# Kernel tuning notes

Measured on AMD Instinct MI355X. Metric: run time of the kernel, lower is better.

The kernel has to match this reference:

```python
import jax, jax.numpy as jnp
import numpy as np
import math

MSG_K = 256  # min(active_count, 256); with uniform(0,1) activations active_count >> 256
N_HEADS = 4
LN_EPS = 1e-5


def _mha(x, wi, bi, wo, bo):
    # torch nn.MultiheadAttention self-attention, batch_first=True
    B, K, D = x.shape
    H = N_HEADS
    hd = D // H
    qkv = x @ wi.T + bi                      # [B,K,3D]
    q, k, v = jnp.split(qkv, 3, axis=-1)
    def split_heads(t):
        return t.reshape(B, K, H, hd).transpose(0, 2, 1, 3)  # [B,H,K,hd]
    q, k, v = split_heads(q), split_heads(k), split_heads(v)
    scores = jnp.einsum('bhqd,bhkd->bhqk', q, k) * (1.0 / math.sqrt(hd))
    attn = jax.nn.softmax(scores, axis=-1)
    o = jnp.einsum('bhqk,bhkd->bhqd', attn, v)
    o = o.transpose(0, 2, 1, 3).reshape(B, K, D)
    return o @ wo.T + bo


def _layernorm(x, g, b):
    mu = jnp.mean(x, axis=-1, keepdims=True)
    var = jnp.mean((x - mu) ** 2, axis=-1, keepdims=True)
    return (x - mu) * jax.lax.rsqrt(var + LN_EPS) * g + b


def setup_inputs() -> dict:
    key = jax.random.key(0)
    ks = jax.random.split(key, 12)
    B, N, D = 32, 4096, 256
    s = 0.02
    return {
        'activation': jax.random.uniform(ks[0], (B, N), dtype=jnp.float32),
        'hidden_state': jax.random.normal(ks[1], (B, N, D), dtype=jnp.float32),
        'in_proj_w': jax.random.normal(ks[2], (3 * D, D), dtype=jnp.float32) * s,
        'in_proj_b': jnp.zeros((3 * D,), jnp.float32),
        'out_proj_w': jax.random.normal(ks[3], (D, D), dtype=jnp.float32) * s,
        'out_proj_b': jnp.zeros((D,), jnp.float32),
        'su_w1': jax.random.normal(ks[4], (D, 2 * D), dtype=jnp.float32) * s,
        'su_b1': jnp.zeros((D,), jnp.float32),
        'su_w2': jax.random.normal(ks[5], (D, D), dtype=jnp.float32) * s,
        'su_b2': jnp.zeros((D,), jnp.float32),
        'au_w1': jax.random.normal(ks[6], (D, 2 * D), dtype=jnp.float32) * s,
        'au_b1': jnp.zeros((D,), jnp.float32),
        'au_w2': jax.random.normal(ks[7], (1, D), dtype=jnp.float32) * s,
        'au_b2': jnp.zeros((1,), jnp.float32),
        'ln_g': jnp.ones((D,), jnp.float32),
        'ln_b': jnp.zeros((D,), jnp.float32),
        'sparsity_k': 256,
    }


def reference(activation, hidden_state, in_proj_w, in_proj_b, out_proj_w, out_proj_b,
              su_w1, su_b1, su_w2, su_b2, au_w1, au_b1, au_w2, au_b2, ln_g, ln_b,
              sparsity_k):
    B, N, D = hidden_state.shape
    b_idx = jnp.arange(B)[:, None]

    # ---- compute_messages: top-k gather -> sparse MHA -> scatter back ----
    topk_vals, topk_idx = jax.lax.top_k(activation, MSG_K)        # [B,K]
    active_states = jnp.take_along_axis(hidden_state, topk_idx[..., None], axis=1)  # [B,K,D]
    msg_sparse = _mha(active_states, in_proj_w, in_proj_b, out_proj_w, out_proj_b)
    msg_sparse = msg_sparse * topk_vals[..., None]
    messages = jnp.zeros((B, N, D), hidden_state.dtype).at[b_idx, topk_idx].set(msg_sparse)

    # ---- update_states: MLP on [old, messages] + LayerNorm ----
    combined = jnp.concatenate([hidden_state, messages], axis=-1)  # [B,N,2D]
    h = jax.nn.gelu(combined @ su_w1.T + su_b1, approximate=False)
    new_hidden = _layernorm(h @ su_w2.T + su_b2, ln_g, ln_b)

    # ---- update_activations ----
    comb2 = jnp.concatenate([hidden_state, new_hidden], axis=-1)
    h2 = jax.nn.gelu(comb2 @ au_w1.T + au_b1, approximate=False)
    delta = jax.nn.sigmoid((h2 @ au_w2.T + au_b2).squeeze(-1))     # [B,N]
    new_activation = jnp.clip(0.7 * activation + 0.3 * delta, 0.0, 1.0)

    # ---- maintain_sparsity: keep top sparsity_k, zero the rest ----
    k = min(int(sparsity_k), N)
    tv, ti = jax.lax.top_k(new_activation, k)                      # [B,k]
    sparse_act = jnp.zeros_like(new_activation).at[b_idx, ti].set(tv)
    kept_hidden = jnp.take_along_axis(new_hidden, ti[..., None], axis=1)
    sparse_hidden = jnp.zeros_like(new_hidden).at[b_idx, ti].set(kept_hidden)
    return sparse_act, sparse_hidden
```

## Files before the change

### kernel.cpp

```cpp
#include <hip/hip_runtime.h>


constexpr int KC = 32;
constexpr int CMAX = 2304;
constexpr float BAND_EPS = 0.004f;
constexpr int MAXBAND = 512;

typedef short bf16x8 __attribute__((ext_vector_type(8)));
typedef float f32x4 __attribute__((ext_vector_type(4)));

__device__ __forceinline__ float gelu_f(float x) {
    return 0.5f * x * (1.0f + erff(x * 0.70710678118654752440f));
}
__device__ __forceinline__ unsigned short f2bf(float f) {
    unsigned u = __float_as_uint(f);
    return (unsigned short)((u + 0x7fffu + ((u >> 16) & 1u)) >> 16);
}
__device__ __forceinline__ float bf2f(unsigned short h) {
    return __uint_as_float(((unsigned)h) << 16);
}
__device__ __forceinline__ int swz(int row, int byteInRow) {
    return (row << 9) + (byteInRow ^ ((row & 7) << 4));
}

__global__ void __launch_bounds__(256) fill0_k(float4* p, long n4) {
    long i = (long)blockIdx.x * 256 + threadIdx.x;
    long stride = (long)gridDim.x * 256;
    float4 z = make_float4(0.f, 0.f, 0.f, 0.f);
    for (; i < n4; i += stride) p[i] = z;
}

__global__ void __launch_bounds__(256) topk1_k(const float* __restrict__ act,
        float* __restrict__ svals, int* __restrict__ sidx, int* __restrict__ cnt)
{
    __shared__ int cs[4];
    __shared__ int sTop, sRest;
    int b = blockIdx.x, tid = threadIdx.x;
    int wid = tid >> 6, lane = tid & 63;
    unsigned v[16];
    #pragma unroll
    for (int s = 0; s < 16; ++s)
        v[s] = __float_as_uint(act[b * 4096 + s * 256 + tid]);

    auto reduce4 = [&](int c) -> int {
        #pragma unroll
        for (int off = 32; off >= 1; off >>= 1) c += __shfl_xor(c, off);
        if (lane == 0) cs[wid] = c;
        __syncthreads();
        int tot = cs[0] + cs[1] + cs[2] + cs[3];
        __syncthreads();
        return tot;
    };
    auto countGE = [&](unsigned thr) -> int {
        int c = 0;
        #pragma unroll
        for (int s = 0; s < 16; ++s) c += (v[s] >= thr) ? 1 : 0;
        return reduce4(c);
    };
    auto countEqLt = [&](unsigned vs, int icut) -> int {
        int c = 0;
        #pragma unroll
        for (int s = 0; s < 16; ++s)
            c += (v[s] == vs && (s * 256 + tid) < icut) ? 1 : 0;
        return reduce4(c);
    };

    unsigned vstar = 0;
    for (int bit = 31; bit >= 0; --bit) {
        unsigned cand = vstar | (1u << bit);
        if (countGE(cand) >= 256) vstar = cand;
    }
    int cgt = countGE(vstar + 1);
    int needed = 256 - cgt;
    int icut = 4096;
    if (countEqLt(vstar, 4096) > needed) {
        int lo = 0, hi = 4096;
        for (int it = 0; it < 12; ++it) {
            int mid = (lo + hi) >> 1;
            if (countEqLt(vstar, mid) <= needed) lo = mid; else hi = mid;
        }
        icut = lo;
    }
    if (tid == 0) { sTop = 0; sRest = 0; }
    __syncthreads();
    float th = __uint_as_float(vstar) - 0.4288f;
    #pragma unroll
    for (int s = 0; s < 16; ++s) {
        int i = s * 256 + tid;
        unsigned vb = v[s];
        float f = __uint_as_float(vb);
        bool top = (vb > vstar) || (vb == vstar && i < icut);
        if (top) {
            int slot = atomicAdd(&sTop, 1);
            sidx[b * 4096 + slot] = i;
            svals[b * 4096 + slot] = f;
        } else if (f >= th) {
            int slot = 256 + atomicAdd(&sRest, 1);
            if (slot < CMAX) {
                sidx[b * 4096 + slot] = i;
                svals[b * 4096 + slot] = f;
            }
        }
    }
    __syncthreads();
    if (tid == 0) cnt[b] = min(256 + sRest, CMAX);
}

__global__ void __launch_bounds__(256) topk2_k(const float* __restrict__ newact,
        const int* __restrict__ sidx, const int* __restrict__ cnt,
        float* __restrict__ selv, int* __restrict__ selo, int* __restrict__ selp)
{
    __shared__ int cs[4];
    __shared__ int sSel;
    int b = blockIdx.x, tid = threadIdx.x;
    int wid = tid >> 6, lane = tid & 63;
    int C = min(cnt[b], CMAX);
    unsigned v[9];
    int org[9];
    #pragma unroll
    for (int s = 0; s < 9; ++s) {
        int p = s * 256 + tid;
        bool ok = (p < C && p < CMAX);
        v[s] = ok ? __float_as_uint(newact[(long)b * CMAX + p]) : 0u;
        org[s] = ok ? sidx[b * 4096 + p] : 0x7FFFFFFF;
    }
    auto reduce4 = [&](int c) -> int {
        #pragma unroll
        for (int off = 32; off >= 1; off >>= 1) c += __shfl_xor(c, off);
        if (lane == 0) cs[wid] = c;
        __syncthreads();
        int tot = cs[0] + cs[1] + cs[2] + cs[3];
        __syncthreads();
        return tot;
    };
    auto countGE = [&](unsigned thr) -> int {
        int c = 0;
        #pragma unroll
        for (int s = 0; s < 9; ++s) c += (v[s] >= thr) ? 1 : 0;
        return reduce4(c);
    };
    auto countEqLt = [&](unsigned vs, int icut) -> int {
        int c = 0;
        #pragma unroll
        for (int s = 0; s < 9; ++s) c += (v[s] == vs && org[s] < icut) ? 1 : 0;
        return reduce4(c);
    };

    unsigned vstar = 0;
    for (int bit = 31; bit >= 0; --bit) {
        unsigned cand = vstar | (1u << bit);
        if (countGE(cand) >= 256) vstar = cand;
    }
    int cgt = countGE(vstar + 1);
    int needed = 256 - cgt;
    int icut = 4096;
    if (countEqLt(vstar, 4096) > needed) {
        int lo = 0, hi = 4096;
        for (int it = 0; it < 12; ++it) {
            int mid = (lo + hi) >> 1;
            if (countEqLt(vstar, mid) <= needed) lo = mid; else hi = mid;
        }
        icut = lo;
    }
    if (tid == 0) sSel = 0;
    __syncthreads();
    #pragma unroll
    for (int s = 0; s < 9; ++s) {
        unsigned vb = v[s];
        bool sel = (vb > vstar) || (vb == vstar && org[s] < icut);
        if (sel) {
            int slot = atomicAdd(&sSel, 1);
            selv[b * 256 + slot] = __uint_as_float(vb);
            selo[b * 256 + slot] = org[s];
            selp[b * 256 + slot] = s * 256 + tid;
        }
    }
}

template<int TM, int TN, int RM, int RN, bool BT, bool GATHER, int EPI>
__global__ void __launch_bounds__(256) gemm_k(
    const float* __restrict__ A, int lda, long sA1, long sA2, int divA,
    const float* __restrict__ B, int ldb, long sB1, long sB2, int divB,
    float* __restrict__ C, int ldc, long sC1, long sC2, int divC,
    int K, const float* __restrict__ bias, const float* __restrict__ rowscale,
    long rsStride, const int* __restrict__ gmap, long gmapStride, float cscale)
{
    constexpr int TX = TN / RN, TY = TM / RM;
    static_assert(TX * TY == 256, "block must be 256 threads");
    __shared__ float As[KC][TM + 4];
    __shared__ float Bs[KC][TN + 4];
    int z = blockIdx.z;
    const float* Ab = A + (long)(z / divA) * sA1 + (long)(z % divA) * sA2;
    const float* Bb = B + (long)(z / divB) * sB1 + (long)(z % divB) * sB2;
    float* Cb = C + (long)(z / divC) * sC1 + (long)(z % divC) * sC2;
    int m0 = blockIdx.y * TM, n0 = blockIdx.x * TN;
    int tid = threadIdx.x;
    int tx = tid % TX, ty = tid / TX;
    float acc[RM][RN];
    #pragma unroll
    for (int i = 0; i < RM; ++i)
        #pragma unroll
        for (int j = 0; j < RN; ++j) acc[i][j] = 0.f;

    for (int k0 = 0; k0 < K; k0 += KC) {
        __syncthreads();
        #pragma unroll
        for (int u = 0; u < (TM * KC) / 1024; ++u) {
            int idx = tid + u * 256;
            int m = idx / (KC / 4), k4 = idx % (KC / 4);
            int row = m0 + m;
            long grow = GATHER ? (long)gmap[(long)z * gmapStride + row] : (long)row;
            float4 v = *(const float4*)(Ab + grow * lda + k0 + k4 * 4);
            As[k4 * 4 + 0][m] = v.x; As[k4 * 4 + 1][m] = v.y;
            As[k4 * 4 + 2][m] = v.z; As[k4 * 4 + 3][m] = v.w;
        }
        if (BT) {
            #pragma unroll
            for (int u = 0; u < (TN * KC) / 1024; ++u) {
                int idx = tid + u * 256;
                int n = idx / (KC / 4), k4 = idx % (KC / 4);
                float4 v = *(const float4*)(Bb + (long)(n0 + n) * ldb + k0 + k4 * 4);
                Bs[k4 * 4 + 0][n] = v.x; Bs[k4 * 4 + 1][n] = v.y;
                Bs[k4 * 4 + 2][n] = v.z; Bs[k4 * 4 + 3][n] = v.w;
            }
        } else {
            #pragma unroll
            for (int u = 0; u < (TN * KC) / 1024; ++u) {
                int idx = tid + u * 256;
                int k = idx / (TN / 4), n4 = idx % (TN / 4);
                float4 v = *(const float4*)(Bb + (long)(k0 + k) * ldb + n0 + n4 * 4);
                *(float4*)&Bs[k][n4 * 4] = v;
            }
        }
        __syncthreads();
        #pragma unroll
        for (int k = 0; k < KC; ++k) {
            float av[RM], bv[RN];
            #pragma unroll
            for (int i = 0; i < RM; i += 4) {
                float4 t = *(const float4*)&As[k][ty * RM + i];
                av[i] = t.x; av[i + 1] = t.y; av[i + 2] = t.z; av[i + 3] = t.w;
            }
            #pragma unroll
            for (int j = 0; j < RN; j += 4) {
                float4 t = *(const float4*)&Bs[k][tx * RN + j];
                bv[j] = t.x; bv[j + 1] = t.y; bv[j + 2] = t.z; bv[j + 3] = t.w;
            }
            #pragma unroll
            for (int i = 0; i < RM; ++i)
                #pragma unroll
                for (int j = 0; j < RN; ++j)
                    acc[i][j] = fmaf(av[i], bv[j], acc[i][j]);
        }
    }
    #pragma unroll
    for (int i = 0; i < RM; ++i) {
        int gm = m0 + ty * RM + i;
        float rs = 1.f;
        if (EPI == 2) rs = rowscale[(long)z * rsStride + gm];
        #pragma unroll
        for (int j = 0; j < RN; j += 4) {
            int gn = n0 + tx * RN + j;
            float4 v = make_float4(acc[i][j], acc[i][j + 1], acc[i][j + 2], acc[i][j + 3]);
            if (EPI == 1 || EPI == 2) {
                float4 bb = *(const float4*)(bias + gn);
                v.x += bb.x; v.y += bb.y; v.z += bb.z; v.w += bb.w;
            }
            if (EPI == 2) { v.x *= rs; v.y *= rs; v.z *= rs; v.w *= rs; }
            if (EPI == 3) { v.x *= cscale; v.y *= cscale; v.z *= cscale; v.w *= cscale; }
            *(float4*)(Cb + (long)gm * ldc + gn) = v;
        }
    }
}

__global__ void __launch_bounds__(256) softmax_k(float* __restrict__ S) {
    int row = blockIdx.x * 4 + (threadIdx.x >> 6);
    int lane = threadIdx.x & 63;
    float4* r = (float4*)(S + (long)row * 256);
    float4 v = r[lane];
    float m = fmaxf(fmaxf(v.x, v.y), fmaxf(v.z, v.w));
    for (int off = 32; off >= 1; off >>= 1) m = fmaxf(m, __shfl_xor(m, off));
    v.x = expf(v.x - m); v.y = expf(v.y - m); v.z = expf(v.z - m); v.w = expf(v.w - m);
    float s = v.x + v.y + v.z + v.w;
    for (int off = 32; off >= 1; off >>= 1) s += __shfl_xor(s, off);
    float inv = 1.f / s;
    v.x *= inv; v.y *= inv; v.z *= inv; v.w *= inv;
    r[lane] = v;
}

__global__ void __launch_bounds__(256) prep_k(
        const float* __restrict__ s1, const float* __restrict__ s2,
        const float* __restrict__ a1,
        unsigned short* __restrict__ o1, unsigned short* __restrict__ o2,
        unsigned short* __restrict__ o3,
        float* __restrict__ w1P, float* __restrict__ w2P, float* __restrict__ auP)
{
    int blk = blockIdx.x, tid = threadIdx.x;
    if (blk < 512) {
        int i = blk * 256 + tid;
        o1[i] = f2bf(s1[i]);
        o3[i] = f2bf(a1[i]);
        if (i < 65536) o2[i] = f2bf(s2[i]);
        return;
    }
    const float* src; float* dst; int ld, ktiles, rel;
    if (blk < 576) { rel = blk - 512; src = s1; ld = 512; dst = w1P; ktiles = 8; }
    else if (blk < 640) { rel = blk - 576; src = s2; ld = 256; dst = w2P; ktiles = 8; }
    else { rel = blk - 640; src = a1; ld = 512; dst = auP; ktiles = 16; }
    int k0 = (rel % ktiles) * 32, n0 = (rel / ktiles) * 32;
    __shared__ float t[32][33];
    int tx = tid & 31, ty = tid >> 5;
    #pragma unroll
    for (int yy = 0; yy < 4; ++yy) {
        int nl = ty * 4 + yy;
        t[nl][tx] = src[(long)(n0 + nl) * ld + k0 + tx];
    }
    __syncthreads();
    #pragma unroll
    for (int yy = 0; yy < 4; ++yy) {
        int k = k0 + ty * 4 + yy;
        dst[(long)(k >> 2) * 1024 + (n0 + tx) * 4 + (k & 3)] = t[tx][ty * 4 + yy];
    }
}

__global__ void __launch_bounds__(256) gatherX_k(const float* __restrict__ hid,
        const int* __restrict__ sidx, const int* __restrict__ cnt,
        unsigned short* __restrict__ Xb)
{
    int b = blockIdx.y;
    int C = min(cnt[b], CMAX);
    int p = blockIdx.x * 4 + (threadIdx.x >> 6);
    int lane = threadIdx.x & 63;
    unsigned short* dst = Xb + ((long)b * CMAX + p) * 256 + lane * 4;
    if (p < C) {
        int row = sidx[b * 4096 + p];
        float4 v = *(const float4*)(hid + ((long)b * 4096 + row) * 256 + lane * 4);
        ushort4 o; o.x = f2bf(v.x); o.y = f2bf(v.y); o.z = f2bf(v.z); o.w = f2bf(v.w);
        *(ushort4*)dst = o;
    } else {
        ushort4 z; z.x = 0; z.y = 0; z.z = 0; z.w = 0;
        *(ushort4*)dst = z;
    }
}

__global__ void __launch_bounds__(256, 2) fused_mlp_k(
    const unsigned short* __restrict__ Xb,
    const unsigned short* __restrict__ W1,
    const unsigned short* __restrict__ W2,
    const unsigned short* __restrict__ WA,
    const float* __restrict__ su_b1v, const float* __restrict__ msgc,
    const float* __restrict__ su_b2v,
    const float* __restrict__ lng, const float* __restrict__ lnb,
    const float* __restrict__ au_b1v,
    const float* __restrict__ w2v, const float* __restrict__ b2s,
    const float* __restrict__ svals, const int* __restrict__ cnt,
    unsigned short* __restrict__ NHb, float* __restrict__ nac)
{
    int b = blockIdx.y;
    int C = min(cnt[b], CMAX);
    int m0 = blockIdx.x * 64;
    if (m0 >= C) return;
    int tid = threadIdx.x;
    int wid = tid >> 6;
    int lane = tid & 63;
    int l15 = lane & 15;
    int q = lane >> 4;
    int n0w = wid * 64;

    __shared__ __align__(16) unsigned short Xs[64 * 256];
    __shared__ __align__(16) unsigned short Hs[64 * 256];
    __shared__ float rsum[4][64];
    __shared__ float rsq[4][64];
    __shared__ float rmu[64], rrs[64];

    const unsigned short* Ab = Xb + ((long)b * CMAX + m0) * 256;

    #pragma unroll
    for (int rnd = 0; rnd < 8; ++rnd) {
        int idx = rnd * 256 + tid;
        int r = idx >> 5, c = idx & 31;
        bf16x8 v = *(const bf16x8*)(Ab + r * 256 + c * 8);
        *(bf16x8*)((char*)Xs + swz(r, c * 16)) = v;
    }
    __syncthreads();

    f32x4 acc[4][4];

    #pragma unroll
    for (int mt = 0; mt < 4; ++mt)
        #pragma unroll
        for (int nt = 0; nt < 4; ++nt) {
            f32x4 z = {0.f, 0.f, 0.f, 0.f};
            acc[mt][nt] = z;
        }
    {
        const unsigned short* wr[4];
        #pragma unroll
        for (int nt = 0; nt < 4; ++nt) wr[nt] = W1 + (long)(n0w + nt * 16 + l15) * 512;
        #pragma unroll 4
        for (int ks = 0; ks < 8; ++ks) {
            int ko = ks * 32;
            bf16x8 af[4], bfr[4];
            #pragma unroll
            for (int mt = 0; mt < 4; ++mt)
                af[mt] = *(const bf16x8*)((const char*)Xs +
                         swz(mt * 16 + l15, (ko + q * 8) * 2));
            #pragma unroll
            for (int nt = 0; nt < 4; ++nt)
                bfr[nt] = *(const bf16x8*)(wr[nt] + ko + q * 8);
            #pragma unroll
            for (int mt = 0; mt < 4; ++mt)
                #pragma unroll
                for (int nt = 0; nt < 4; ++nt)
                    acc[mt][nt] = __builtin_amdgcn_mfma_f32_16x16x32_bf16(
                        af[mt], bfr[nt], acc[mt][nt], 0, 0, 0);
        }
        float bb[4];
        #pragma unroll
        for (int nt = 0; nt < 4; ++nt) bb[nt] = su_b1v[n0w + nt * 16 + l15];
        #pragma unroll
        for (int mt = 0; mt < 4; ++mt) {
            #pragma unroll
            for (int reg = 0; reg < 4; ++reg) {
                int lr = mt * 16 + q * 4 + reg;
                int p = m0 + lr;
                const float* mrow = msgc + ((long)b * 256 + p) * 256;
                bool hasm = (p < 256);
                #pragma unroll
                for (int nt = 0; nt < 4; ++nt) {
                    int gc = n0w + nt * 16 + l15;
                    float v = acc[mt][nt][reg] + bb[nt];
                    if (hasm) v += mrow[gc];
                    *(unsigned short*)((char*)Hs + swz(lr, gc * 2)) = f2bf(gelu_f(v));
                }
            }
        }
    }
    __syncthreads();

    #pragma unroll
    for (int mt = 0; mt < 4; ++mt)
        #pragma unroll
        for (int nt = 0; nt < 4; ++nt) {
            f32x4 z = {0.f, 0.f, 0.f, 0.f};
            acc[mt][nt] = z;
        }
    {
        const unsigned short* wr[4];
        #pragma unroll
        for (int nt = 0; nt < 4; ++nt) wr[nt] = W2 + (long)(n0w + nt * 16 + l15) * 256;
        #pragma unroll
        for (int ks = 0; ks < 8; ++ks) {
            int ko = ks * 32;
            bf16x8 af[4], bfr[4];
            #pragma unroll
            for (int mt = 0; mt < 4; ++mt) {
                int r = mt * 16 + l15;
                af[mt] = *(const bf16x8*)((const char*)Hs + swz(r, (ko + q * 8) * 2));
            }
            #pragma unroll
            for (int nt = 0; nt < 4; ++nt)
                bfr[nt] = *(const bf16x8*)(wr[nt] + ko + q * 8);
            #pragma unroll
            for (int mt = 0; mt < 4; ++mt)
                #pragma unroll
                for (int nt = 0; nt < 4; ++nt)
                    acc[mt][nt] = __builtin_amdgcn_mfma_f32_16x16x32_bf16(
                        af[mt], bfr[nt], acc[mt][nt], 0, 0, 0);
        }
        float bb[4], gg[4], eb[4];
        #pragma unroll
        for (int nt = 0; nt < 4; ++nt) {
            int gc = n0w + nt * 16 + l15;
            bb[nt] = su_b2v[gc]; gg[nt] = lng[gc]; eb[nt] = lnb[gc];
        }
        #pragma unroll
        for (int mt = 0; mt < 4; ++mt)
            #pragma unroll
            for (int nt = 0; nt < 4; ++nt)
                #pragma unroll
                for (int reg = 0; reg < 4; ++reg)
                    acc[mt][nt][reg] += bb[nt];
        #pragma unroll
        for (int mt = 0; mt < 4; ++mt) {
            #pragma unroll
            for (int reg = 0; reg < 4; ++reg) {
                float s = 0.f, s2 = 0.f;
                #pragma unroll
                for (int nt = 0; nt < 4; ++nt) {
                    float v = acc[mt][nt][reg];
                    s += v; s2 += v * v;
                }
                #pragma unroll
                for (int off = 1; off <= 8; off <<= 1) {
                    s += __shfl_xor(s, off);
                    s2 += __shfl_xor(s2, off);
                }
                if (l15 == 0) {
                    int row = mt * 16 + q * 4 + reg;
                    rsum[wid][row] = s; rsq[wid][row] = s2;
                }
            }
        }
        __syncthreads();
        if (tid < 64) {
            float s = rsum[0][tid] + rsum[1][tid] + rsum[2][tid] + rsum[3][tid];
            float s2 = rsq[0][tid] + rsq[1][tid] + rsq[2][tid] + rsq[3][tid];
            float mu = s * (1.f / 256.f);
            float var = s2 * (1.f / 256.f) - mu * mu;
            rmu[tid] = mu;
            rrs[tid] = rsqrtf(var + 1e-5f);
        }
        __syncthreads();
        #pragma unroll
        for (int mt = 0; mt < 4; ++mt) {
            #pragma unroll
            for (int reg = 0; reg < 4; ++reg) {
                int lr = mt * 16 + q * 4 + reg;
                float mu = rmu[lr], rs = rrs[lr];
                #pragma unroll
                for (int nt = 0; nt < 4; ++nt) {
                    int gc = n0w + nt * 16 + l15;
                    unsigned short ov =
                        f2bf((acc[mt][nt][reg] - mu) * rs * gg[nt] + eb[nt]);
                    *(unsigned short*)((char*)Hs + swz(lr, gc * 2)) = ov;
                }
            }
        }
    }
    __syncthreads();

    #pragma unroll
    for (int rnd = 0; rnd < 8; ++rnd) {
        int idx = rnd * 256 + tid;
        int r = idx >> 5, c = idx & 31;
        bf16x8 v = *(const bf16x8*)((const char*)Hs + swz(r, c * 16));
        *(bf16x8*)(NHb + ((long)b * CMAX + m0 + r) * 256 + c * 8) = v;
    }

    #pragma unroll
    for (int mt = 0; mt < 4; ++mt)
        #pragma unroll
        for (int nt = 0; nt < 4; ++nt) {
            f32x4 z = {0.f, 0.f, 0.f, 0.f};
            acc[mt][nt] = z;
        }
    {
        const unsigned short* wr[4];
        #pragma unroll
        for (int nt = 0; nt < 4; ++nt) wr[nt] = WA + (long)(n0w + nt * 16 + l15) * 512;
        #pragma unroll 4
        for (int ks = 0; ks < 8; ++ks) {
            int ko = ks * 32;
            bf16x8 af[4], bfr[4];
            #pragma unroll
            for (int mt = 0; mt < 4; ++mt)
                af[mt] = *(const bf16x8*)((const char*)Xs +
                         swz(mt * 16 + l15, (ko + q * 8) * 2));
            #pragma unroll
            for (int nt = 0; nt < 4; ++nt)
                bfr[nt] = *(const bf16x8*)(wr[nt] + ko + q * 8);
            #pragma unroll
            for (int mt = 0; mt < 4; ++mt)
                #pragma unroll
                for (int nt = 0; nt < 4; ++nt)
                    acc[mt][nt] = __builtin_amdgcn_mfma_f32_16x16x32_bf16(
                        af[mt], bfr[nt], acc[mt][nt], 0, 0, 0);
        }
        #pragma unroll
        for (int ks = 0; ks < 8; ++ks) {
            int ko = ks * 32;
            int kw = 256 + ks * 32;
            bf16x8 af[4], bfr[4];
            #pragma unroll
            for (int mt = 0; mt < 4; ++mt) {
                int r = mt * 16 + l15;
                af[mt] = *(const bf16x8*)((const char*)Hs + swz(r, (ko + q * 8) * 2));
            }
            #pragma unroll
            for (int nt = 0; nt < 4; ++nt)
                bfr[nt] = *(const bf16x8*)(wr[nt] + kw + q * 8);
            #pragma unroll
            for (int mt = 0; mt < 4; ++mt)
                #pragma unroll
                for (int nt = 0; nt < 4; ++nt)
                    acc[mt][nt] = __builtin_amdgcn_mfma_f32_16x16x32_bf16(
                        af[mt], bfr[nt], acc[mt][nt], 0, 0, 0);
        }
        float bb[4], ww[4];
        #pragma unroll
        for (int nt = 0; nt < 4; ++nt) {
            int gc = n0w + nt * 16 + l15;
            bb[nt] = au_b1v[gc]; ww[nt] = w2v[gc];
        }
        #pragma unroll
        for (int mt = 0; mt < 4; ++mt) {
            #pragma unroll
            for (int reg = 0; reg < 4; ++reg) {
                float s = 0.f;
                #pragma unroll
                for (int nt = 0; nt < 4; ++nt)
                    s += gelu_f(acc[mt][nt][reg] + bb[nt]) * ww[nt];
                #pragma unroll
                for (int off = 1; off <= 8; off <<= 1) s += __shfl_xor(s, off);
                if (l15 == 0) rsum[wid][mt * 16 + q * 4 + reg] = s;
            }
        }
        __syncthreads();
        if (tid < 64) {
            int p = m0 + tid;
            if (p < C) {
                float z = rsum[0][tid] + rsum[1][tid] + rsum[2][tid] + rsum[3][tid] + b2s[0];
                float delta = 1.f / (1.f + expf(-z));
                float na = 0.7f * svals[b * 4096 + p] + 0.3f * delta;
                nac[(long)b * CMAX + p] = fminf(fmaxf(na, 0.f), 1.f);
            }
        }
    }
}

__global__ void __launch_bounds__(256) selectT_k(const float* __restrict__ nac,
        const int* __restrict__ cnt, float* __restrict__ T)
{
    __shared__ float v[CMAX];
    __shared__ int cs[256];
    __shared__ float bounds[2];
    int b = blockIdx.x, tid = threadIdx.x;
    int C = min(cnt[b], CMAX);
    for (int i = tid; i < CMAX; i += 256)
        v[i] = (i < C) ? nac[(long)b * CMAX + i] : -1.f;
    if (tid == 0) { bounds[0] = 0.f; bounds[1] = 1.0f; }
    __syncthreads();
    for (int it = 0; it < 20; ++it) {
        float mid = 0.5f * (bounds[0] + bounds[1]);
        int c = 0;
        for (int i = tid; i < CMAX; i += 256) c += (v[i] >= mid) ? 1 : 0;
        cs[tid] = c; __syncthreads();
        for (int s = 128; s; s >>= 1) {
            if (tid < s) cs[tid] += cs[tid + s];
            __syncthreads();
        }
        if (tid == 0) { if (cs[0] >= 256) bounds[0] = mid; else bounds[1] = mid; }
        __syncthreads();
    }
    if (tid == 0) T[b] = bounds[0];
}

__global__ void __launch_bounds__(256) bandlist_k(const float* __restrict__ nac,
        const int* __restrict__ cnt, const float* __restrict__ Tarr,
        int* __restrict__ bandlist, int* __restrict__ bandcnt)
{
    int b = blockIdx.y;
    int C = min(cnt[b], CMAX);
    int p = blockIdx.x * 256 + threadIdx.x;
    if (p < C && fabsf(nac[(long)b * CMAX + p] - Tarr[b]) < BAND_EPS) {
        int slot = atomicAdd(&bandcnt[b], 1);
        if (slot < MAXBAND) bandlist[b * MAXBAND + slot] = p;
    }
}

__global__ void __launch_bounds__(256) bandfix_k(
    const float* __restrict__ hid, const int* __restrict__ sidx,
    const float* __restrict__ msgc,
    const float* __restrict__ w1Pf, const float* __restrict__ su_b1,
    const float* __restrict__ w2Pf, const float* __restrict__ su_b2,
    const float* __restrict__ ln_g, const float* __restrict__ ln_b,
    const float* __restrict__ auPf, const float* __restrict__ au_b1,
    const float* __restrict__ au_w2, const float* __restrict__ au_b2,
    const float* __restrict__ svals,
    const int* __restrict__ bandlist, const int* __restrict__ bandcnt,
    float* __restrict__ nac, unsigned short* __restrict__ NHb)
{
    int b = blockIdx.y;
    int M = min(bandcnt[b], MAXBAND);
    int base = blockIdx.x * 4;
    if (base >= M) return;
    int nact = min(M - base, 4);
    int tid = threadIdx.x;
    int wid = tid >> 6, lane = tid & 63;
    const float4* w1P = (const float4*)w1Pf;
    const float4* w2P = (const float4*)w2Pf;
    const float4* auP = (const float4*)auPf;
    __shared__ float xr[4][256];
    __shared__ float hy[4][256];
    __shared__ float nh[4][256];
    __shared__ float muS[4], rsS[4];
    __shared__ int ppS[4];
    if (tid < 4)
        ppS[tid] = (tid < nact) ? bandlist[b * MAXBAND + base + tid] : -1;
    __syncthreads();
    #pragma unroll
    for (int r = 0; r < 4; ++r) {
        int pp = ppS[r];
        xr[r][tid] = (pp >= 0) ? hid[((long)b * 4096 + sidx[b * 4096 + pp]) * 256 + tid] : 0.f;
    }
    __syncthreads();
    int n = tid;
    float acc[4];
    #pragma unroll
    for (int r = 0; r < 4; ++r) acc[r] = 0.f;
    for (int k4 = 0; k4 < 64; ++k4) {
        float4 w = w1P[k4 * 256 + n];
        #pragma unroll
        for (int r = 0; r < 4; ++r) {
            float4 xv = *(const float4*)&xr[r][k4 * 4];
            acc[r] = fmaf(w.x, xv.x, acc[r]);
            acc[r] = fmaf(w.y, xv.y, acc[r]);
            acc[r] = fmaf(w.z, xv.z, acc[r]);
            acc[r] = fmaf(w.w, xv.w, acc[r]);
        }
    }
    float b1v = su_b1[n];
    #pragma unroll
    for (int r = 0; r < 4; ++r) {
        int pp = ppS[r];
        float s = acc[r] + b1v;
        if (pp >= 0 && pp < 256) s += msgc[((long)b * 256 + pp) * 256 + n];
        acc[r] = gelu_f(s);
    }
    __syncthreads();
    #pragma unroll
    for (int r = 0; r < 4; ++r) hy[r][n] = acc[r];
    __syncthreads();
    #pragma unroll
    for (int r = 0; r < 4; ++r) acc[r] = 0.f;
    for (int k4 = 0; k4 < 64; ++k4) {
        float4 w = w2P[k4 * 256 + n];
        #pragma unroll
        for (int r = 0; r < 4; ++r) {
            float4 hv = *(const float4*)&hy[r][k4 * 4];
            acc[r] = fmaf(w.x, hv.x, acc[r]);
            acc[r] = fmaf(w.y, hv.y, acc[r]);
            acc[r] = fmaf(w.z, hv.z, acc[r]);
            acc[r] = fmaf(w.w, hv.w, acc[r]);
        }
    }
    __syncthreads();
    float b2v = su_b2[n];
    #pragma unroll
    for (int r = 0; r < 4; ++r) hy[r][n] = acc[r] + b2v;
    __syncthreads();
    {
        int r = wid;
        float4 yv = *(const float4*)&hy[r][lane * 4];
        float s = yv.x + yv.y + yv.z + yv.w;
        float s2 = yv.x * yv.x + yv.y * yv.y + yv.z * yv.z + yv.w * yv.w;
        #pragma unroll
        for (int off = 32; off >= 1; off >>= 1) {
            s += __shfl_xor(s, off);
            s2 += __shfl_xor(s2, off);
        }
        if (lane == 0) {
            float mu = s * (1.f / 256.f);
            float var = s2 * (1.f / 256.f) - mu * mu;
            muS[r] = mu; rsS[r] = rsqrtf(var + 1e-5f);
        }
    }
    __syncthreads();
    float gv = ln_g[n], ev = ln_b[n];
    #pragma unroll
    for (int r = 0; r < 4; ++r) {
        float o = (hy[r][n] - muS[r]) * rsS[r] * gv + ev;
        nh[r][n] = o;
        if (ppS[r] >= 0) NHb[((long)b * CMAX + ppS[r]) * 256 + n] = f2bf(o);
    }
    __syncthreads();
    #pragma unroll
    for (int r = 0; r < 4; ++r) acc[r] = 0.f;
    for (int k4 = 0; k4 < 64; ++k4) {
        float4 w = auP[k4 * 256 + n];
        #pragma unroll
        for (int r = 0; r < 4; ++r) {
            float4 xv = *(const float4*)&xr[r][k4 * 4];
            acc[r] = fmaf(w.x, xv.x, acc[r]);
            acc[r] = fmaf(w.y, xv.y, acc[r]);
            acc[r] = fmaf(w.z, xv.z, acc[r]);
            acc[r] = fmaf(w.w, xv.w, acc[r]);
        }
    }
    for (int k4 = 64; k4 < 128; ++k4) {
        float4 w = auP[k4 * 256 + n];
        #pragma unroll
        for (int r = 0; r < 4; ++r) {
            float4 hv = *(const float4*)&nh[r][(k4 - 64) * 4];
            acc[r] = fmaf(w.x, hv.x, acc[r]);
            acc[r] = fmaf(w.y, hv.y, acc[r]);
            acc[r] = fmaf(w.z, hv.z, acc[r]);
            acc[r] = fmaf(w.w, hv.w, acc[r]);
        }
    }
    float ab = au_b1[n], wv2 = au_w2[n];
    __syncthreads();
    #pragma unroll
    for (int r = 0; r < 4; ++r) hy[r][n] = gelu_f(acc[r] + ab) * wv2;
    __syncthreads();
    {
        int r = wid;
        float4 gvv = *(const float4*)&hy[r][lane * 4];
        float s = gvv.x + gvv.y + gvv.z + gvv.w;
        #pragma unroll
        for (int off = 32; off >= 1; off >>= 1) s += __shfl_xor(s, off);
        if (lane == 0 && ppS[r] >= 0) {
            float z = s + au_b2[0];
            float delta = 1.f / (1.f + expf(-z));
            float na = 0.7f * svals[b * 4096 + ppS[r]] + 0.3f * delta;
            nac[(long)b * CMAX + ppS[r]] = fminf(fmaxf(na, 0.f), 1.f);
        }
    }
}

__global__ void __launch_bounds__(64) scatter_k(const float* __restrict__ selv,
        const int* __restrict__ selo, const int* __restrict__ selp,
        const unsigned short* __restrict__ NHb, float* __restrict__ out)
{
    int b = blockIdx.x >> 8, j = blockIdx.x & 255, t = threadIdx.x;
    int orig = selo[b * 256 + j];
    int p = selp[b * 256 + j];
    if (t == 0) out[b * 4096 + orig] = selv[b * 256 + j];
    const ushort4* src = (const ushort4*)(NHb + ((long)b * CMAX + p) * 256);
    ushort4 s = src[t];
    float4 o = make_float4(bf2f(s.x), bf2f(s.y), bf2f(s.z), bf2f(s.w));
    *(float4*)(out + 131072 + ((long)(b * 4096 + orig)) * 256 + t * 4) = o;
}

extern "C" void kernel_launch(void* const* d_in, const int* in_sizes, int n_in,
                              void* d_out, int out_size, void* d_ws, size_t ws_size,
                              hipStream_t stream)
{
    const float* act   = (const float*)d_in[0];
    const float* hid   = (const float*)d_in[1];
    const float* wi    = (const float*)d_in[2];
    const float* bi    = (const float*)d_in[3];
    const float* wo    = (const float*)d_in[4];
    const float* bo    = (const float*)d_in[5];
    const float* su_w1 = (const float*)d_in[6];
    const float* su_b1 = (const float*)d_in[7];
    const float* su_w2 = (const float*)d_in[8];
    const float* su_b2 = (const float*)d_in[9];
    const float* au_w1 = (const float*)d_in[10];
    const float* au_b1 = (const float*)d_in[11];
    const float* au_w2 = (const float*)d_in[12];
    const float* au_b2 = (const float*)d_in[13];
    const float* ln_g  = (const float*)d_in[14];
    const float* ln_b  = (const float*)d_in[15];
    float* out = (float*)d_out;

    char* ws = (char*)d_ws;
    size_t off = 0;
    auto alloc = [&](size_t bytes) {
        size_t o = off; off += (bytes + 255) & ~(size_t)255; return o;
    };
    float* svals = (float*)(ws + alloc((size_t)32 * 4096 * 4));
    int*   sidx  = (int*)  (ws + alloc((size_t)32 * 4096 * 4));
    int*   cnt   = (int*)  (ws + alloc(256));
    float* qkv   = (float*)(ws + alloc((size_t)32 * 256 * 768 * 4));
    float* Sb    = (float*)(ws + alloc((size_t)32 * 4 * 256 * 256 * 4));
    float* Ob    = (float*)(ws + alloc((size_t)32 * 256 * 256 * 4));
    float* MSG   = (float*)(ws + alloc((size_t)32 * 256 * 256 * 4));
    float* MSGC  = (float*)(ws + alloc((size_t)32 * 256 * 256 * 4));
    float* selv  = (float*)(ws + alloc((size_t)32 * 256 * 4));
    int*   selo  = (int*)  (ws + alloc((size_t)32 * 256 * 4));
    int*   selp  = (int*)  (ws + alloc((size_t)32 * 256 * 4));
    unsigned short* swb1 = (unsigned short*)(ws + alloc((size_t)256 * 512 * 2));
    unsigned short* swb2 = (unsigned short*)(ws + alloc((size_t)256 * 256 * 2));
    unsigned short* awb1 = (unsigned short*)(ws + alloc((size_t)256 * 512 * 2));
    float* w1P = (float*)(ws + alloc((size_t)256 * 256 * 4));
    float* w2P = (float*)(ws + alloc((size_t)256 * 256 * 4));
    float* auP = (float*)(ws + alloc((size_t)512 * 256 * 4));
    unsigned short* Xb   = (unsigned short*)(ws + alloc((size_t)32 * CMAX * 256 * 2));
    unsigned short* NHb  = (unsigned short*)(ws + alloc((size_t)32 * CMAX * 256 * 2));
    float* nac = (float*)(ws + alloc((size_t)32 * CMAX * 4));
    float* Tb  = (float*)(ws + alloc(128));
    int* bandl = (int*)(ws + alloc((size_t)32 * MAXBAND * 4));
    int* bandc = (int*)(ws + alloc(128));

    hipMemsetAsync(bandc, 0, 32 * sizeof(int), stream);
    fill0_k<<<2048, 256, 0, stream>>>((float4*)out, (long)out_size / 4);
    topk1_k<<<32, 256, 0, stream>>>(act, svals, sidx, cnt);
    prep_k<<<768, 256, 0, stream>>>(su_w1, su_w2, au_w1, swb1, swb2, awb1,
                                    w1P, w2P, auP);
    gatherX_k<<<dim3(CMAX / 4, 32), 256, 0, stream>>>(hid, sidx, cnt, Xb);
    gemm_k<64, 256, 8, 8, true, true, 1><<<dim3(3, 4, 32), 256, 0, stream>>>(
        hid, 256, (long)4096 * 256, 0, 1,
        wi, 256, 0, 0, 1,
        qkv, 768, (long)256 * 768, 0, 1,
        256, bi, nullptr, 0, sidx, 4096, 0.f);
    gemm_k<64, 256, 8, 8, true, false, 3><<<dim3(1, 4, 128), 256, 0, stream>>>(
        qkv, 768, 196608, 64, 4,
        qkv + 256, 768, 196608, 64, 4,
        Sb, 256, 65536, 0, 1,
        64, nullptr, nullptr, 0, nullptr, 0, 0.125f);
    softmax_k<<<8192, 256, 0, stream>>>(Sb);
    gemm_k<64, 64, 4, 4, false, false, 0><<<dim3(1, 4, 128), 256, 0, stream>>>(
        Sb, 256, 65536, 0, 1,
        qkv + 512, 768, 196608, 64, 4,
        Ob, 256, 65536, 64, 4,
        256, nullptr, nullptr, 0, nullptr, 0, 0.f);
    gemm_k<64, 256, 8, 8, true, false, 2><<<dim3(1, 4, 32), 256, 0, stream>>>(
        Ob, 256, 65536, 0, 1,
        wo, 256, 0, 0, 1,
        MSG, 256, 65536, 0, 1,
        256, bo, svals, 4096, nullptr, 0, 0.f);
    gemm_k<64, 256, 8, 8, true, false, 0><<<dim3(1, 4, 32), 256, 0, stream>>>(
        MSG, 256, 65536, 0, 1,
        su_w1 + 256, 512, 0, 0, 1,
        MSGC, 256, 65536, 0, 1,
        256, nullptr, nullptr, 0, nullptr, 0, 0.f);
    fused_mlp_k<<<dim3(CMAX / 64, 32), 256, 0, stream>>>(Xb, swb1, swb2, awb1,
        su_b1, MSGC, su_b2, ln_g, ln_b, au_b1, au_w2, au_b2, svals, cnt,
        NHb, nac);
    selectT_k<<<32, 256, 0, stream>>>(nac, cnt, Tb);
    bandlist_k<<<dim3(CMAX / 256, 32), 256, 0, stream>>>(nac, cnt, Tb, bandl, bandc);
    bandfix_k<<<dim3(MAXBAND / 4, 32), 256, 0, stream>>>(hid, sidx, MSGC,
        w1P, su_b1, w2P, su_b2, ln_g, ln_b, auP, au_b1, au_w2, au_b2,
        svals, bandl, bandc, nac, NHb);
    topk2_k<<<32, 256, 0, stream>>>(nac, sidx, cnt, selv, selo, selp);
    scatter_k<<<8192, 64, 0, stream>>>(selv, selo, selp, NHb, out);
}
```

Baseline: 726.4 us.

## Halve fused MLP row tile and fuse both X-side GEMMs into one pass

The fused MLP kernel now processes 32 rows per block instead of 64, which halves shared memory and doubles the grid. Occupancy hint rises from 2 to 3 blocks per CU. The hidden_state half of the activation-update GEMM is computed in the first loop, sharing the X fragment loads with the state-update GEMM, so the separate later X pass goes away. The trade-off is that each weight tile is now reused across fewer rows, so global or L2 weight traffic per row doubles, and register pressure grows from holding two accumulator sets.

```diff
diff --git a/kernel.cpp b/kernel.cpp
--- a/kernel.cpp
+++ b/kernel.cpp
@@ -343,7 +343,7 @@
     }
 }
 
-__global__ void __launch_bounds__(256, 2) fused_mlp_k(
+__global__ void __launch_bounds__(256, 3) fused_mlp_k(
     const unsigned short* __restrict__ Xb,
     const unsigned short* __restrict__ W1,
     const unsigned short* __restrict__ W2,
@@ -358,7 +358,7 @@
 {
     int b = blockIdx.y;
     int C = min(cnt[b], CMAX);
-    int m0 = blockIdx.x * 64;
+    int m0 = blockIdx.x * 32;
     if (m0 >= C) return;
     int tid = threadIdx.x;
     int wid = tid >> 6;
@@ -367,16 +367,16 @@
     int q = lane >> 4;
     int n0w = wid * 64;
 
-    __shared__ __align__(16) unsigned short Xs[64 * 256];
-    __shared__ __align__(16) unsigned short Hs[64 * 256];
-    __shared__ float rsum[4][64];
-    __shared__ float rsq[4][64];
-    __shared__ float rmu[64], rrs[64];
+    __shared__ __align__(16) unsigned short Xs[32 * 256];
+    __shared__ __align__(16) unsigned short Hs[32 * 256];
+    __shared__ float rsum[4][32];
+    __shared__ float rsq[4][32];
+    __shared__ float rmu[32], rrs[32];
 
     const unsigned short* Ab = Xb + ((long)b * CMAX + m0) * 256;
 
     #pragma unroll
-    for (int rnd = 0; rnd < 8; ++rnd) {
+    for (int rnd = 0; rnd < 4; ++rnd) {
         int idx = rnd * 256 + tid;
         int r = idx >> 5, c = idx & 31;
         bf16x8 v = *(const bf16x8*)(Ab + r * 256 + c * 8);
@@ -384,42 +384,53 @@
     }
     __syncthreads();
 
-    f32x4 acc[4][4];
-
-    #pragma unroll
-    for (int mt = 0; mt < 4; ++mt)
+    f32x4 accA[2][4];
+    f32x4 accX[2][4];
+    #pragma unroll
+    for (int mt = 0; mt < 2; ++mt)
         #pragma unroll
         for (int nt = 0; nt < 4; ++nt) {
             f32x4 z = {0.f, 0.f, 0.f, 0.f};
-            acc[mt][nt] = z;
-        }
+            accA[mt][nt] = z; accX[mt][nt] = z;
+        }
+
     {
-        const unsigned short* wr[4];
-        #pragma unroll
-        for (int nt = 0; nt < 4; ++nt) wr[nt] = W1 + (long)(n0w + nt * 16 + l15) * 512;
+        const unsigned short* wrA[4];
+        const unsigned short* wrX[4];
+        #pragma unroll
+        for (int nt = 0; nt < 4; ++nt) {
+            long rowoff = (long)(n0w + nt * 16 + l15) * 512;
+            wrA[nt] = W1 + rowoff;
+            wrX[nt] = WA + rowoff;
+        }
         #pragma unroll 4
         for (int ks = 0; ks < 8; ++ks) {
             int ko = ks * 32;
-            bf16x8 af[4], bfr[4];
-            #pragma unroll
-            for (int mt = 0; mt < 4; ++mt)
+            bf16x8 af[2], bfrA[4], bfrX[4];
+            #pragma unroll
+            for (int mt = 0; mt < 2; ++mt)
                 af[mt] = *(const bf16x8*)((const char*)Xs +
                          swz(mt * 16 + l15, (ko + q * 8) * 2));
             #pragma unroll
-            for (int nt = 0; nt < 4; ++nt)
-                bfr[nt] = *(const bf16x8*)(wr[nt] + ko + q * 8);
-            #pragma unroll
-            for (int mt = 0; mt < 4; ++mt)
-                #pragma unroll
-                for (int nt = 0; nt < 4; ++nt)
-                    acc[mt][nt] = __builtin_amdgcn_mfma_f32_16x16x32_bf16(
-                        af[mt], bfr[nt], acc[mt][nt], 0, 0, 0);
+            for (int nt = 0; nt < 4; ++nt) {
+                bfrA[nt] = *(const bf16x8*)(wrA[nt] + ko + q * 8);
+                bfrX[nt] = *(const bf16x8*)(wrX[nt] + ko + q * 8);
+            }
+            #pragma unroll
+            for (int mt = 0; mt < 2; ++mt)
+                #pragma unroll
+                for (int nt = 0; nt < 4; ++nt) {
+                    accA[mt][nt] = __builtin_amdgcn_mfma_f32_16x16x32_bf16(
+                        af[mt], bfrA[nt], accA[mt][nt], 0, 0, 0);
+                    accX[mt][nt] = __builtin_amdgcn_mfma_f32_16x16x32_bf16(
+                        af[mt], bfrX[nt], accX[mt][nt], 0, 0, 0);
+                }
         }
         float bb[4];
         #pragma unroll
         for (int nt = 0; nt < 4; ++nt) bb[nt] = su_b1v[n0w + nt * 16 + l15];
         #pragma unroll
-        for (int mt = 0; mt < 4; ++mt) {
+        for (int mt = 0; mt < 2; ++mt) {
             #pragma unroll
             for (int reg = 0; reg < 4; ++reg) {
                 int lr = mt * 16 + q * 4 + reg;
@@ -429,7 +440,7 @@
                 #pragma unroll
                 for (int nt = 0; nt < 4; ++nt) {
                     int gc = n0w + nt * 16 + l15;
-                    float v = acc[mt][nt][reg] + bb[nt];
+                    float v = accA[mt][nt][reg] + bb[nt];
                     if (hasm) v += mrow[gc];
                     *(unsigned short*)((char*)Hs + swz(lr, gc * 2)) = f2bf(gelu_f(v));
                 }
@@ -439,11 +450,11 @@
     __syncthreads();
 
     #pragma unroll
-    for (int mt = 0; mt < 4; ++mt)
+    for (int mt = 0; mt < 2; ++mt)
         #pragma unroll
         for (int nt = 0; nt < 4; ++nt) {
             f32x4 z = {0.f, 0.f, 0.f, 0.f};
-            acc[mt][nt] = z;
+            accA[mt][nt] = z;
         }
     {
         const unsigned short* wr[4];
@@ -452,9 +463,9 @@
         #pragma unroll
         for (int ks = 0; ks < 8; ++ks) {
             int ko = ks * 32;
-            bf16x8 af[4], bfr[4];
-            #pragma unroll
-            for (int mt = 0; mt < 4; ++mt) {
+            bf16x8 af[2], bfr[4];
+            #pragma unroll
+            for (int mt = 0; mt < 2; ++mt) {
                 int r = mt * 16 + l15;
                 af[mt] = *(const bf16x8*)((const char*)Hs + swz(r, (ko + q * 8) * 2));
             }
@@ -462,11 +473,11 @@
             for (int nt = 0; nt < 4; ++nt)
                 bfr[nt] = *(const bf16x8*)(wr[nt] + ko + q * 8);
             #pragma unroll
-            for (int mt = 0; mt < 4; ++mt)
+            for (int mt = 0; mt < 2; ++mt)
                 #pragma unroll
                 for (int nt = 0; nt < 4; ++nt)
-                    acc[mt][nt] = __builtin_amdgcn_mfma_f32_16x16x32_bf16(
-                        af[mt], bfr[nt], acc[mt][nt], 0, 0, 0);
+                    accA[mt][nt] = __builtin_amdgcn_mfma_f32_16x16x32_bf16(
+                        af[mt], bfr[nt], accA[mt][nt], 0, 0, 0);
         }
         float bb[4], gg[4], eb[4];
         #pragma unroll
@@ -475,20 +486,20 @@
             bb[nt] = su_b2v[gc]; gg[nt] = lng[gc]; eb[nt] = lnb[gc];
         }
         #pragma unroll
-        for (int mt = 0; mt < 4; ++mt)
+        for (int mt = 0; mt < 2; ++mt)
             #pragma unroll
             for (int nt = 0; nt < 4; ++nt)
                 #pragma unroll
                 for (int reg = 0; reg < 4; ++reg)
-                    acc[mt][nt][reg] += bb[nt];
-        #pragma unroll
-        for (int mt = 0; mt < 4; ++mt) {
+                    accA[mt][nt][reg] += bb[nt];
+        #pragma unroll
+        for (int mt = 0; mt < 2; ++mt) {
             #pragma unroll
             for (int reg = 0; reg < 4; ++reg) {
                 float s = 0.f, s2 = 0.f;
                 #pragma unroll
                 for (int nt = 0; nt < 4; ++nt) {
-                    float v = acc[mt][nt][reg];
+                    float v = accA[mt][nt][reg];
                     s += v; s2 += v * v;
                 }
                 #pragma unroll
@@ -503,7 +514,7 @@
             }
         }
         __syncthreads();
-        if (tid < 64) {
+        if (tid < 32) {
             float s = rsum[0][tid] + rsum[1][tid] + rsum[2][tid] + rsum[3][tid];
             float s2 = rsq[0][tid] + rsq[1][tid] + rsq[2][tid] + rsq[3][tid];
             float mu = s * (1.f / 256.f);
@@ -513,7 +524,7 @@
         }
         __syncthreads();
         #pragma unroll
-        for (int mt = 0; mt < 4; ++mt) {
+        for (int mt = 0; mt < 2; ++mt) {
             #pragma unroll
             for (int reg = 0; reg < 4; ++reg) {
                 int lr = mt * 16 + q * 4 + reg;
@@ -522,7 +533,7 @@
                 for (int nt = 0; nt < 4; ++nt) {
                     int gc = n0w + nt * 16 + l15;
                     unsigned short ov =
-                        f2bf((acc[mt][nt][reg] - mu) * rs * gg[nt] + eb[nt]);
+                        f2bf((accA[mt][nt][reg] - mu) * rs * gg[nt] + eb[nt]);
                     *(unsigned short*)((char*)Hs + swz(lr, gc * 2)) = ov;
                 }
             }
@@ -531,61 +542,36 @@
     __syncthreads();
 
     #pragma unroll
-    for (int rnd = 0; rnd < 8; ++rnd) {
+    for (int rnd = 0; rnd < 4; ++rnd) {
         int idx = rnd * 256 + tid;
         int r = idx >> 5, c = idx & 31;
         bf16x8 v = *(const bf16x8*)((const char*)Hs + swz(r, c * 16));
         *(bf16x8*)(NHb + ((long)b * CMAX + m0 + r) * 256 + c * 8) = v;
     }
 
-    #pragma unroll
-    for (int mt = 0; mt < 4; ++mt)
-        #pragma unroll
-        for (int nt = 0; nt < 4; ++nt) {
-            f32x4 z = {0.f, 0.f, 0.f, 0.f};
-            acc[mt][nt] = z;
-        }
     {
         const unsigned short* wr[4];
         #pragma unroll
-        for (int nt = 0; nt < 4; ++nt) wr[nt] = WA + (long)(n0w + nt * 16 + l15) * 512;
-        #pragma unroll 4
+        for (int nt = 0; nt < 4; ++nt)
+            wr[nt] = WA + (long)(n0w + nt * 16 + l15) * 512 + 256;
+        #pragma unroll
         for (int ks = 0; ks < 8; ++ks) {
             int ko = ks * 32;
-            bf16x8 af[4], bfr[4];
-            #pragma unroll
-            for (int mt = 0; mt < 4; ++mt)
-                af[mt] = *(const bf16x8*)((const char*)Xs +
-                         swz(mt * 16 + l15, (ko + q * 8) * 2));
+            bf16x8 af[2], bfr[4];
+            #pragma unroll
+            for (int mt = 0; mt < 2; ++mt) {
+                int r = mt * 16 + l15;
+                af[mt] = *(const bf16x8*)((const char*)Hs + swz(r, (ko + q * 8) * 2));
+            }
             #pragma unroll
             for (int nt = 0; nt < 4; ++nt)
                 bfr[nt] = *(const bf16x8*)(wr[nt] + ko + q * 8);
             #pragma unroll
-            for (int mt = 0; mt < 4; ++mt)
+            for (int mt = 0; mt < 2; ++mt)
                 #pragma unroll
                 for (int nt = 0; nt < 4; ++nt)
-                    acc[mt][nt] = __builtin_amdgcn_mfma_f32_16x16x32_bf16(
-                        af[mt], bfr[nt], acc[mt][nt], 0, 0, 0);
-        }
-        #pragma unroll
-        for (int ks = 0; ks < 8; ++ks) {
-            int ko = ks * 32;
-            int kw = 256 + ks * 32;
-            bf16x8 af[4], bfr[4];
-            #pragma unroll
-            for (int mt = 0; mt < 4; ++mt) {
-                int r = mt * 16 + l15;
-                af[mt] = *(const bf16x8*)((const char*)Hs + swz(r, (ko + q * 8) * 2));
-            }
-            #pragma unroll
-            for (int nt = 0; nt < 4; ++nt)
-                bfr[nt] = *(const bf16x8*)(wr[nt] + kw + q * 8);
-            #pragma unroll
-            for (int mt = 0; mt < 4; ++mt)
-                #pragma unroll
-                for (int nt = 0; nt < 4; ++nt)
-                    acc[mt][nt] = __builtin_amdgcn_mfma_f32_16x16x32_bf16(
-                        af[mt], bfr[nt], acc[mt][nt], 0, 0, 0);
+                    accX[mt][nt] = __builtin_amdgcn_mfma_f32_16x16x32_bf16(
+                        af[mt], bfr[nt], accX[mt][nt], 0, 0, 0);
         }
         float bb[4], ww[4];
         #pragma unroll
@@ -594,20 +580,20 @@
             bb[nt] = au_b1v[gc]; ww[nt] = w2v[gc];
         }
         #pragma unroll
-        for (int mt = 0; mt < 4; ++mt) {
+        for (int mt = 0; mt < 2; ++mt) {
             #pragma unroll
             for (int reg = 0; reg < 4; ++reg) {
                 float s = 0.f;
                 #pragma unroll
                 for (int nt = 0; nt < 4; ++nt)
-                    s += gelu_f(acc[mt][nt][reg] + bb[nt]) * ww[nt];
+                    s += gelu_f(accX[mt][nt][reg] + bb[nt]) * ww[nt];
                 #pragma unroll
                 for (int off = 1; off <= 8; off <<= 1) s += __shfl_xor(s, off);
                 if (l15 == 0) rsum[wid][mt * 16 + q * 4 + reg] = s;
             }
         }
         __syncthreads();
-        if (tid < 64) {
+        if (tid < 32) {
             int p = m0 + tid;
             if (p < C) {
                 float z = rsum[0][tid] + rsum[1][tid] + rsum[2][tid] + rsum[3][tid] + b2s[0];
@@ -906,7 +892,7 @@
         su_w1 + 256, 512, 0, 0, 1,
         MSGC, 256, 65536, 0, 1,
         256, nullptr, nullptr, 0, nullptr, 0, 0.f);
-    fused_mlp_k<<<dim3(CMAX / 64, 32), 256, 0, stream>>>(Xb, swb1, swb2, awb1,
+    fused_mlp_k<<<dim3(CMAX / 32, 32), 256, 0, stream>>>(Xb, swb1, swb2, awb1,
         su_b1, MSGC, su_b2, ln_g, ln_b, au_b1, au_w2, au_b2, svals, cnt,
         NHb, nac);
     selectT_k<<<32, 256, 0, stream>>>(nac, cnt, Tb);
```

Result: slower. 742.5 us (+2.2%).

## Fuse softmax into score GEMM epilogue and chain out-proj with message projection

Applied to the files above, without the earlier changes.

The separate softmax kernel is removed and row softmax is computed in the score GEMM's register epilogue with 32-lane shuffles, since each block holds full 256-wide rows. The out-projection GEMM and the su_w1 message-half GEMM are merged into one kernel that keeps the scaled message tile in shared memory, so the MSG intermediate is never written to or read from global memory. This saves two launches and several round trips of 8 MB buffers, but the merged kernel uses a smaller 32-row tile with a large shared buffer and launches only 256 blocks, which may lower occupancy.

```diff
diff --git a/kernel.cpp b/kernel.cpp
--- a/kernel.cpp
+++ b/kernel.cpp
@@ -187,6 +187,7 @@
 {
     constexpr int TX = TN / RN, TY = TM / RM;
     static_assert(TX * TY == 256, "block must be 256 threads");
+    static_assert(EPI != 4 || TX == 32, "softmax epilogue needs TX==32");
     __shared__ float As[KC][TM + 4];
     __shared__ float Bs[KC][TN + 4];
     int z = blockIdx.z;
@@ -253,6 +254,30 @@
                     acc[i][j] = fmaf(av[i], bv[j], acc[i][j]);
         }
     }
+    if (EPI == 4) {
+        #pragma unroll
+        for (int i = 0; i < RM; ++i) {
+            float m = -1e30f;
+            #pragma unroll
+            for (int j = 0; j < RN; ++j) {
+                acc[i][j] *= cscale;
+                m = fmaxf(m, acc[i][j]);
+            }
+            #pragma unroll
+            for (int off = 16; off >= 1; off >>= 1) m = fmaxf(m, __shfl_xor(m, off));
+            float s = 0.f;
+            #pragma unroll
+            for (int j = 0; j < RN; ++j) {
+                acc[i][j] = expf(acc[i][j] - m);
+                s += acc[i][j];
+            }
+            #pragma unroll
+            for (int off = 16; off >= 1; off >>= 1) s += __shfl_xor(s, off);
+            float inv = 1.f / s;
+            #pragma unroll
+            for (int j = 0; j < RN; ++j) acc[i][j] *= inv;
+        }
+    }
     #pragma unroll
     for (int i = 0; i < RM; ++i) {
         int gm = m0 + ty * RM + i;
@@ -273,19 +298,127 @@
     }
 }
 
-__global__ void __launch_bounds__(256) softmax_k(float* __restrict__ S) {
-    int row = blockIdx.x * 4 + (threadIdx.x >> 6);
-    int lane = threadIdx.x & 63;
-    float4* r = (float4*)(S + (long)row * 256);
-    float4 v = r[lane];
-    float m = fmaxf(fmaxf(v.x, v.y), fmaxf(v.z, v.w));
-    for (int off = 32; off >= 1; off >>= 1) m = fmaxf(m, __shfl_xor(m, off));
-    v.x = expf(v.x - m); v.y = expf(v.y - m); v.z = expf(v.z - m); v.w = expf(v.w - m);
-    float s = v.x + v.y + v.z + v.w;
-    for (int off = 32; off >= 1; off >>= 1) s += __shfl_xor(s, off);
-    float inv = 1.f / s;
-    v.x *= inv; v.y *= inv; v.z *= inv; v.w *= inv;
-    r[lane] = v;
+__global__ void __launch_bounds__(256) msgc_k(
+    const float* __restrict__ Ob,
+    const float* __restrict__ wo,
+    const float* __restrict__ bo,
+    const float* __restrict__ su_w1,
+    const float* __restrict__ svals,
+    float* __restrict__ MSGC)
+{
+    constexpr int TM = 32, TN = 256, RM = 4, RN = 8;
+    constexpr int TX = TN / RN;
+    __shared__ float As[KC][TM + 4];
+    __shared__ float Bs[KC][TN + 4];
+    __shared__ float Ms[TM][TN + 4];
+    int b = blockIdx.y;
+    int m0 = blockIdx.x * TM;
+    int tid = threadIdx.x;
+    int tx = tid % TX, ty = tid / TX;
+    const float* Ab = Ob + (long)b * 65536;
+    float acc[RM][RN];
+
+    #pragma unroll
+    for (int i = 0; i < RM; ++i)
+        #pragma unroll
+        for (int j = 0; j < RN; ++j) acc[i][j] = 0.f;
+    for (int k0 = 0; k0 < 256; k0 += KC) {
+        __syncthreads();
+        {
+            int m = tid / (KC / 4), k4 = tid % (KC / 4);
+            float4 v = *(const float4*)(Ab + (long)(m0 + m) * 256 + k0 + k4 * 4);
+            As[k4 * 4 + 0][m] = v.x; As[k4 * 4 + 1][m] = v.y;
+            As[k4 * 4 + 2][m] = v.z; As[k4 * 4 + 3][m] = v.w;
+        }
+        #pragma unroll
+        for (int u = 0; u < 8; ++u) {
+            int idx = tid + u * 256;
+            int n = idx / (KC / 4), k4 = idx % (KC / 4);
+            float4 v = *(const float4*)(wo + (long)n * 256 + k0 + k4 * 4);
+            Bs[k4 * 4 + 0][n] = v.x; Bs[k4 * 4 + 1][n] = v.y;
+            Bs[k4 * 4 + 2][n] = v.z; Bs[k4 * 4 + 3][n] = v.w;
+        }
+        __syncthreads();
+        #pragma unroll
+        for (int k = 0; k < KC; ++k) {
+            float av[RM], bv[RN];
+            float4 ta = *(const float4*)&As[k][ty * RM];
+            av[0] = ta.x; av[1] = ta.y; av[2] = ta.z; av[3] = ta.w;
+            #pragma unroll
+            for (int j = 0; j < RN; j += 4) {
+                float4 t = *(const float4*)&Bs[k][tx * RN + j];
+                bv[j] = t.x; bv[j + 1] = t.y; bv[j + 2] = t.z; bv[j + 3] = t.w;
+            }
+            #pragma unroll
+            for (int i = 0; i < RM; ++i)
+                #pragma unroll
+                for (int j = 0; j < RN; ++j)
+                    acc[i][j] = fmaf(av[i], bv[j], acc[i][j]);
+        }
+    }
+    __syncthreads();
+    #pragma unroll
+    for (int i = 0; i < RM; ++i) {
+        int gm = m0 + ty * RM + i;
+        float tv = svals[b * 4096 + gm];
+        #pragma unroll
+        for (int j = 0; j < RN; j += 4) {
+            int gn = tx * RN + j;
+            float4 bb = *(const float4*)(bo + gn);
+            float4 v;
+            v.x = (acc[i][j + 0] + bb.x) * tv;
+            v.y = (acc[i][j + 1] + bb.y) * tv;
+            v.z = (acc[i][j + 2] + bb.z) * tv;
+            v.w = (acc[i][j + 3] + bb.w) * tv;
+            *(float4*)&Ms[ty * RM + i][gn] = v;
+        }
+    }
+
+    #pragma unroll
+    for (int i = 0; i < RM; ++i)
+        #pragma unroll
+        for (int j = 0; j < RN; ++j) acc[i][j] = 0.f;
+    const float* W1b = su_w1 + 256;
+    for (int k0 = 0; k0 < 256; k0 += KC) {
+        __syncthreads();
+        #pragma unroll
+        for (int u = 0; u < 8; ++u) {
+            int idx = tid + u * 256;
+            int n = idx / (KC / 4), k4 = idx % (KC / 4);
+            float4 v = *(const float4*)(W1b + (long)n * 512 + k0 + k4 * 4);
+            Bs[k4 * 4 + 0][n] = v.x; Bs[k4 * 4 + 1][n] = v.y;
+            Bs[k4 * 4 + 2][n] = v.z; Bs[k4 * 4 + 3][n] = v.w;
+        }
+        __syncthreads();
+        #pragma unroll
+        for (int k = 0; k < KC; ++k) {
+            float av[RM], bv[RN];
+            #pragma unroll
+            for (int i = 0; i < RM; ++i)
+                av[i] = Ms[ty * RM + i][k0 + k];
+            #pragma unroll
+            for (int j = 0; j < RN; j += 4) {
+                float4 t = *(const float4*)&Bs[k][tx * RN + j];
+                bv[j] = t.x; bv[j + 1] = t.y; bv[j + 2] = t.z; bv[j + 3] = t.w;
+            }
+            #pragma unroll
+            for (int i = 0; i < RM; ++i)
+                #pragma unroll
+                for (int j = 0; j < RN; ++j)
+                    acc[i][j] = fmaf(av[i], bv[j], acc[i][j]);
+        }
+    }
+    float* Cb = MSGC + (long)b * 65536;
+    #pragma unroll
+    for (int i = 0; i < RM; ++i) {
+        int gm = m0 + ty * RM + i;
+        #pragma unroll
+        for (int j = 0; j < RN; j += 4) {
+            int gn = tx * RN + j;
+            float4 v = make_float4(acc[i][j], acc[i][j + 1], acc[i][j + 2], acc[i][j + 3]);
+            *(float4*)(Cb + (long)gm * 256 + gn) = v;
+        }
+    }
 }
 
 __global__ void __launch_bounds__(256) prep_k(
@@ -856,7 +989,6 @@
     float* qkv   = (float*)(ws + alloc((size_t)32 * 256 * 768 * 4));
     float* Sb    = (float*)(ws + alloc((size_t)32 * 4 * 256 * 256 * 4));
     float* Ob    = (float*)(ws + alloc((size_t)32 * 256 * 256 * 4));
-    float* MSG   = (float*)(ws + alloc((size_t)32 * 256 * 256 * 4));
     float* MSGC  = (float*)(ws + alloc((size_t)32 * 256 * 256 * 4));
     float* selv  = (float*)(ws + alloc((size_t)32 * 256 * 4));
     int*   selo  = (int*)  (ws + alloc((size_t)32 * 256 * 4));
@@ -885,27 +1017,17 @@
         wi, 256, 0, 0, 1,
         qkv, 768, (long)256 * 768, 0, 1,
         256, bi, nullptr, 0, sidx, 4096, 0.f);
-    gemm_k<64, 256, 8, 8, true, false, 3><<<dim3(1, 4, 128), 256, 0, stream>>>(
+    gemm_k<64, 256, 8, 8, true, false, 4><<<dim3(1, 4, 128), 256, 0, stream>>>(
         qkv, 768, 196608, 64, 4,
         qkv + 256, 768, 196608, 64, 4,
         Sb, 256, 65536, 0, 1,
         64, nullptr, nullptr, 0, nullptr, 0, 0.125f);
-    softmax_k<<<8192, 256, 0, stream>>>(Sb);
     gemm_k<64, 64, 4, 4, false, false, 0><<<dim3(1, 4, 128), 256, 0, stream>>>(
         Sb, 256, 65536, 0, 1,
         qkv + 512, 768, 196608, 64, 4,
         Ob, 256, 65536, 64, 4,
         256, nullptr, nullptr, 0, nullptr, 0, 0.f);
-    gemm_k<64, 256, 8, 8, true, false, 2><<<dim3(1, 4, 32), 256, 0, stream>>>(
-        Ob, 256, 65536, 0, 1,
-        wo, 256, 0, 0, 1,
-        MSG, 256, 65536, 0, 1,
-        256, bo, svals, 4096, nullptr, 0, 0.f);
-    gemm_k<64, 256, 8, 8, true, false, 0><<<dim3(1, 4, 32), 256, 0, stream>>>(
-        MSG, 256, 65536, 0, 1,
-        su_w1 + 256, 512, 0, 0, 1,
-        MSGC, 256, 65536, 0, 1,
-        256, nullptr, nullptr, 0, nullptr, 0, 0.f);
+    msgc_k<<<dim3(8, 32), 256, 0, stream>>>(Ob, wo, bo, su_w1, svals, MSGC);
     fused_mlp_k<<<dim3(CMAX / 64, 32), 256, 0, stream>>>(Xb, swb1, swb2, awb1,
         su_b1, MSGC, su_b2, ln_g, ln_b, au_b1, au_w2, au_b2, svals, cnt,
         NHb, nac);
```

After: 698.7 us. -3.8%, faster.
